# Kernel optimization log

Measured on AMD Instinct MI355X. Metric: run time of the kernel, lower is better.

Reference implementation:

```python
import jax, jax.numpy as jnp
import numpy as np

MEM = 2048

def _linear_params(key, scale):
    kw, kb = jax.random.split(key)
    W = jax.random.uniform(kw, (MEM, MEM), jnp.float32, -scale, scale)
    b = jax.random.uniform(kb, (MEM,), jnp.float32, -scale, scale)
    return W, b

def setup_inputs() -> dict:
    key = jax.random.key(0)
    ks = jax.random.split(key, 18)
    scale = 1.0 / np.sqrt(MEM)
    inp = {
        'lc': jax.random.normal(ks[0], (1, MEM), jnp.float32),
        'lh': jax.random.normal(ks[1], (1, MEM), jnp.float32),
        'rc': jax.random.normal(ks[2], (1, MEM), jnp.float32),
        'rh': jax.random.normal(ks[3], (1, MEM), jnp.float32),
        'S': jax.random.normal(ks[4], (1, MEM), jnp.float32),
        'w': jax.random.normal(ks[5], (1, MEM), jnp.float32),
    }
    names = ['Wh', 'Us', 'ma', 'ilh', 'irh', 'lflh', 'lfrh', 'rflh', 'rfrh', 'ulh', 'urh']
    for i, n in enumerate(names):
        W, b = _linear_params(ks[6 + i], scale)
        inp[n + '_w'] = W
        inp[n + '_b'] = b
    return inp

def _lin(x, W, b):
    return x @ W.T + b

def reference(lc, lh, rc, rh, S, w,
              Wh_w, Wh_b, Us_w, Us_b, ma_w, ma_b,
              ilh_w, ilh_b, irh_w, irh_b,
              lflh_w, lflh_b, lfrh_w, lfrh_b,
              rflh_w, rflh_b, rfrh_w, rfrh_b,
              ulh_w, ulh_b, urh_w, urh_b):
    # attention scoring over the two children
    m_left = jnp.tanh(_lin(lh, Wh_w, Wh_b) + _lin(S, Us_w, Us_b)).squeeze()   # [MEM]
    m_right = jnp.tanh(_lin(rh, Wh_w, Wh_b) + _lin(S, Us_w, Us_b)).squeeze()  # [MEM]
    exp_left = w @ m_left[:, None]    # [1,1]
    exp_right = w @ m_right[:, None]  # [1,1]
    denom = exp_left + exp_right
    left_alpha = exp_left / denom
    right_alpha = exp_right / denom
    # attention-weighted child hidden states
    la = jnp.tanh(_lin(left_alpha * lh, ma_w, ma_b))   # [1,MEM]
    ra = jnp.tanh(_lin(right_alpha * rh, ma_w, ma_b))  # [1,MEM]
    # tree-LSTM gates
    i = jax.nn.sigmoid(_lin(la, ilh_w, ilh_b) + _lin(ra, irh_w, irh_b))
    lf = jax.nn.sigmoid(_lin(la, lflh_w, lflh_b) + _lin(ra, lfrh_w, lfrh_b))
    rf = jax.nn.sigmoid(_lin(la, rflh_w, rflh_b) + _lin(ra, rfrh_w, rfrh_b))
    update = jnp.tanh(_lin(la, ulh_w, ulh_b) + _lin(ra, urh_w, urh_b))
    c = i * update + lf * lc + rf * rc
    h = jnp.tanh(c)
    return (c, h)
```

## Files before the change

kernel.cpp:

```cpp
#include <hip/hip_runtime.h>
#include <hip/hip_bf16.h>
#include <math.h>

#define MEM 2048
#define NF4 512

__device__ __forceinline__ float dot4(float4 a, float4 b) {
    return a.x * b.x + a.y * b.y + a.z * b.z + a.w * b.w;
}

__device__ __forceinline__ float wave_reduce(float v) {
#pragma unroll
    for (int off = 32; off > 0; off >>= 1)
        v += __shfl_down(v, off, 64);
    return v;
}

__device__ __forceinline__ float sigmoidf_(float x) {
    return 1.0f / (1.0f + expf(-x));
}


__global__ __launch_bounds__(256) void
k1_slab(const float* __restrict__ lh, const float* __restrict__ rh,
        const float* __restrict__ S,
        const float* __restrict__ Wh_w, const float* __restrict__ Us_w,
        const float* __restrict__ ma_w,
        float* __restrict__ ws)
{
    __shared__ __align__(16) float s_x1[MEM];
    __shared__ __align__(16) float s_x2[MEM];

    const int t  = threadIdx.x;
    const int m  = blockIdx.y;
    const int rg = blockIdx.x;

    const float* W  = (m == 0) ? Wh_w : (m == 1) ? Us_w : ma_w;
    const float* x1 = (m == 1) ? S : lh;
    const float* x2 = (m == 1) ? S : rh;

    {
        const float4* a4 = (const float4*)x1;
        const float4* b4 = (const float4*)x2;
        float4* s14 = (float4*)s_x1;
        float4* s24 = (float4*)s_x2;
        for (int i = t; i < NF4; i += 256) { s14[i] = a4[i]; s24[i] = b4[i]; }
    }
    __syncthreads();

    const int wv = t >> 6, ln = t & 63;
    const int row0 = rg * 8 + wv * 2;

    const float4* __restrict__ w0 = (const float4*)(W + (size_t)row0 * MEM);
    const float4* __restrict__ w1 = w0 + NF4;
    const float4* sx1 = (const float4*)s_x1;
    const float4* sx2 = (const float4*)s_x2;

    float a00 = 0.f, a01 = 0.f, a10 = 0.f, a11 = 0.f;
#pragma unroll
    for (int i = 0; i < 8; ++i) {
        const int idx = i * 64 + ln;
        const float4 wa = w0[idx];
        const float4 wb = w1[idx];
        const float4 p  = sx1[idx];
        const float4 q  = sx2[idx];
        a00 += dot4(wa, p); a01 += dot4(wa, q);
        a10 += dot4(wb, p); a11 += dot4(wb, q);
    }
    a00 = wave_reduce(a00); a01 = wave_reduce(a01);
    a10 = wave_reduce(a10); a11 = wave_reduce(a11);

    if (ln == 0) {
        if (m == 0) {
            ws[row0] = a00; ws[row0 + 1] = a10;
            ws[MEM + row0] = a01; ws[MEM + row0 + 1] = a11;
        } else if (m == 1) {
            ws[2 * MEM + row0] = a00; ws[2 * MEM + row0 + 1] = a10;
        } else {
            ws[3 * MEM + row0] = a00; ws[3 * MEM + row0 + 1] = a10;
            ws[4 * MEM + row0] = a01; ws[4 * MEM + row0 + 1] = a11;
        }
    }
}

__global__ __launch_bounds__(1024) void
k_mid(const float* __restrict__ w, const float* __restrict__ Wh_b,
      const float* __restrict__ Us_b, const float* __restrict__ ma_b,
      float* __restrict__ ws)
{
    __shared__ float s_red[16][2];
    __shared__ float s_al[2];

    const int t = threadIdx.x;
    float el = 0.f, er = 0.f;
    for (int j = t; j < MEM; j += 1024) {
        const float us = ws[2 * MEM + j] + Us_b[j];
        const float bb = Wh_b[j] + us;
        const float ml = tanhf(ws[j] + bb);
        const float mr = tanhf(ws[MEM + j] + bb);
        const float wj = w[j];
        el += wj * ml; er += wj * mr;
    }
    el = wave_reduce(el);
    er = wave_reduce(er);
    const int wv = t >> 6, ln = t & 63;
    if (ln == 0) { s_red[wv][0] = el; s_red[wv][1] = er; }
    __syncthreads();
    if (t == 0) {
        float e0 = 0.f, e1 = 0.f;
#pragma unroll
        for (int k = 0; k < 16; ++k) { e0 += s_red[k][0]; e1 += s_red[k][1]; }
        const float d = e0 + e1;
        s_al[0] = e0 / d;
        s_al[1] = e1 / d;
    }
    __syncthreads();
    const float al = s_al[0];
    const float ar = s_al[1];
    for (int j = t; j < MEM; j += 1024) {
        const float mb = ma_b[j];
        const float la = tanhf(al * ws[3 * MEM + j] + mb);
        const float ra = tanhf(ar * ws[4 * MEM + j] + mb);
        ws[j] = la;
        ws[MEM + j] = ra;
    }
}

__global__ __launch_bounds__(256) void
k2_slab(const float* __restrict__ ilh_w,  const float* __restrict__ irh_w,
        const float* __restrict__ lflh_w, const float* __restrict__ lfrh_w,
        const float* __restrict__ rflh_w, const float* __restrict__ rfrh_w,
        const float* __restrict__ ulh_w,  const float* __restrict__ urh_w,
        float* __restrict__ ws)
{
    __shared__ __align__(16) float s_x[MEM];

    const int t  = threadIdx.x;
    const int m  = blockIdx.y;
    const int rg = blockIdx.x;

    const float* Wt[8] = {ilh_w, irh_w, lflh_w, lfrh_w, rflh_w, rfrh_w, ulh_w, urh_w};
    const float* W = Wt[m];
    const float* x = ws + (size_t)(m & 1) * MEM;

    {
        const float4* x4 = (const float4*)x;
        float4* s4 = (float4*)s_x;
        for (int i = t; i < NF4; i += 256) s4[i] = x4[i];
    }
    __syncthreads();

    const int wv = t >> 6, ln = t & 63;
    const int row0 = rg * 8 + wv * 2;

    const float4* __restrict__ w0 = (const float4*)(W + (size_t)row0 * MEM);
    const float4* __restrict__ w1 = w0 + NF4;
    const float4* sx = (const float4*)s_x;

    float a0 = 0.f, a1 = 0.f;
#pragma unroll
    for (int i = 0; i < 8; ++i) {
        const int idx = i * 64 + ln;
        const float4 wa = w0[idx];
        const float4 wb = w1[idx];
        const float4 xv = sx[idx];
        a0 += dot4(wa, xv);
        a1 += dot4(wb, xv);
    }
    a0 = wave_reduce(a0);
    a1 = wave_reduce(a1);
    if (ln == 0) {
        float* p = ws + (size_t)(2 + m) * MEM;
        p[row0]     = a0;
        p[row0 + 1] = a1;
    }
}

__global__ __launch_bounds__(256) void
k3_combine(const float* __restrict__ lc, const float* __restrict__ rc,
           const float* __restrict__ ilh_b,  const float* __restrict__ irh_b,
           const float* __restrict__ lflh_b, const float* __restrict__ lfrh_b,
           const float* __restrict__ rflh_b, const float* __restrict__ rfrh_b,
           const float* __restrict__ ulh_b,  const float* __restrict__ urh_b,
           const float* __restrict__ ws, float* __restrict__ out)
{
    const int j = blockIdx.x * 256 + threadIdx.x;
    const float* P = ws + 2 * MEM;
    const float gi = sigmoidf_(P[j]           + P[MEM + j]     + ilh_b[j]  + irh_b[j]);
    const float lf = sigmoidf_(P[2 * MEM + j] + P[3 * MEM + j] + lflh_b[j] + lfrh_b[j]);
    const float rf = sigmoidf_(P[4 * MEM + j] + P[5 * MEM + j] + rflh_b[j] + rfrh_b[j]);
    const float u  = tanhf(    P[6 * MEM + j] + P[7 * MEM + j] + ulh_b[j]  + urh_b[j]);
    const float c  = gi * u + lf * lc[j] + rf * rc[j];
    out[j]       = c;
    out[MEM + j] = tanhf(c);
}

extern "C" void kernel_launch(void* const* d_in, const int* in_sizes, int n_in,
                              void* d_out, int out_size, void* d_ws, size_t ws_size,
                              hipStream_t stream) {
    const float* lc = (const float*)d_in[0];
    const float* lh = (const float*)d_in[1];
    const float* rc = (const float*)d_in[2];
    const float* rh = (const float*)d_in[3];
    const float* S  = (const float*)d_in[4];
    const float* w  = (const float*)d_in[5];
    const float* Wh_w   = (const float*)d_in[6];   const float* Wh_b   = (const float*)d_in[7];
    const float* Us_w   = (const float*)d_in[8];   const float* Us_b   = (const float*)d_in[9];
    const float* ma_w   = (const float*)d_in[10];  const float* ma_b   = (const float*)d_in[11];
    const float* ilh_w  = (const float*)d_in[12];  const float* ilh_b  = (const float*)d_in[13];
    const float* irh_w  = (const float*)d_in[14];  const float* irh_b  = (const float*)d_in[15];
    const float* lflh_w = (const float*)d_in[16];  const float* lflh_b = (const float*)d_in[17];
    const float* lfrh_w = (const float*)d_in[18];  const float* lfrh_b = (const float*)d_in[19];
    const float* rflh_w = (const float*)d_in[20];  const float* rflh_b = (const float*)d_in[21];
    const float* rfrh_w = (const float*)d_in[22];  const float* rfrh_b = (const float*)d_in[23];
    const float* ulh_w  = (const float*)d_in[24];  const float* ulh_b  = (const float*)d_in[25];
    const float* urh_w  = (const float*)d_in[26];  const float* urh_b  = (const float*)d_in[27];

    float* out = (float*)d_out;
    float* ws  = (float*)d_ws;

    dim3 g1(256, 3);
    k1_slab<<<g1, 256, 0, stream>>>(lh, rh, S, Wh_w, Us_w, ma_w, ws);

    k_mid<<<1, 1024, 0, stream>>>(w, Wh_b, Us_b, ma_b, ws);

    dim3 g2(256, 8);
    k2_slab<<<g2, 256, 0, stream>>>(ilh_w, irh_w, lflh_w, lfrh_w,
                                    rflh_w, rfrh_w, ulh_w, urh_w, ws);

    k3_combine<<<8, 256, 0, stream>>>(lc, rc, ilh_b, irh_b, lflh_b, lfrh_b,
                                      rflh_b, rfrh_b, ulh_b, urh_b, ws, out);
}
```

Baseline: 251.3 us.

## Stream weight rows through LDS via async global_load_lds triple buffering

Both matvec kernels now fetch weight rows with global_load_lds straight into a per-wave triple-buffered LDS staging area. Explicit vmcnt waits keep two chunks in flight while the current chunk is consumed. Previously all eight unrolled global loads could already be issued up front, so the aim is mainly to cut register pressure and VGPR round trips. The cost is extra LDS traffic, 24KB more shared memory per block (which may reduce occupancy), and reliance on hand-set wait counts with no barrier.

```diff
diff --git a/kernel.cpp b/kernel.cpp
--- a/kernel.cpp
+++ b/kernel.cpp
@@ -1,6 +1,7 @@
 #include <hip/hip_runtime.h>
 #include <hip/hip_bf16.h>
 #include <math.h>
+#include <stdint.h>
 
 #define MEM 2048
 #define NF4 512
@@ -18,6 +19,18 @@
 
 __device__ __forceinline__ float sigmoidf_(float x) {
     return 1.0f / (1.0f + expf(-x));
+}
+
+__device__ __forceinline__ void dma16(const float* g, float* l) {
+    __builtin_amdgcn_global_load_lds(
+        (const __attribute__((address_space(1))) uint32_t*)(uintptr_t)(const void*)g,
+        (__attribute__((address_space(3))) uint32_t*)(uintptr_t)(const void*)l,
+        16, 0, 0);
+}
+
+template <int N>
+__device__ __forceinline__ void wait_vmcnt() {
+    asm volatile("s_waitcnt vmcnt(%0)" ::"n"(N) : "memory");
 }
 
 
@@ -30,6 +43,7 @@
 {
     __shared__ __align__(16) float s_x1[MEM];
     __shared__ __align__(16) float s_x2[MEM];
+    __shared__ __align__(16) float s_stg[4][3][2][256];
 
     const int t  = threadIdx.x;
     const int m  = blockIdx.y;
@@ -51,19 +65,35 @@
     const int wv = t >> 6, ln = t & 63;
     const int row0 = rg * 8 + wv * 2;
 
-    const float4* __restrict__ w0 = (const float4*)(W + (size_t)row0 * MEM);
-    const float4* __restrict__ w1 = w0 + NF4;
+    const float* g0 = W + (size_t)row0 * MEM + ln * 4;
+    const float* g1 = g0 + MEM;
+
+    dma16(g0 + 0 * 256, &s_stg[wv][0][0][0]);
+    dma16(g1 + 0 * 256, &s_stg[wv][0][1][0]);
+    dma16(g0 + 1 * 256, &s_stg[wv][1][0][0]);
+    dma16(g1 + 1 * 256, &s_stg[wv][1][1][0]);
+
     const float4* sx1 = (const float4*)s_x1;
     const float4* sx2 = (const float4*)s_x2;
 
     float a00 = 0.f, a01 = 0.f, a10 = 0.f, a11 = 0.f;
 #pragma unroll
-    for (int i = 0; i < 8; ++i) {
-        const int idx = i * 64 + ln;
-        const float4 wa = w0[idx];
-        const float4 wb = w1[idx];
-        const float4 p  = sx1[idx];
-        const float4 q  = sx2[idx];
+    for (int c = 0; c < 8; ++c) {
+        if (c + 2 < 8) {
+            const int nb = (c + 2) % 3;
+            dma16(g0 + (c + 2) * 256, &s_stg[wv][nb][0][0]);
+            dma16(g1 + (c + 2) * 256, &s_stg[wv][nb][1][0]);
+            wait_vmcnt<4>();
+        } else if (c + 1 < 8) {
+            wait_vmcnt<2>();
+        } else {
+            wait_vmcnt<0>();
+        }
+        const int buf = c % 3;
+        const float4 wa = ((const float4*)&s_stg[wv][buf][0][0])[ln];
+        const float4 wb = ((const float4*)&s_stg[wv][buf][1][0])[ln];
+        const float4 p  = sx1[c * 64 + ln];
+        const float4 q  = sx2[c * 64 + ln];
         a00 += dot4(wa, p); a01 += dot4(wa, q);
         a10 += dot4(wb, p); a11 += dot4(wb, q);
     }
@@ -134,6 +164,7 @@
         float* __restrict__ ws)
 {
     __shared__ __align__(16) float s_x[MEM];
+    __shared__ __align__(16) float s_stg[4][3][2][256];
 
     const int t  = threadIdx.x;
     const int m  = blockIdx.y;
@@ -153,17 +184,33 @@
     const int wv = t >> 6, ln = t & 63;
     const int row0 = rg * 8 + wv * 2;
 
-    const float4* __restrict__ w0 = (const float4*)(W + (size_t)row0 * MEM);
-    const float4* __restrict__ w1 = w0 + NF4;
+    const float* g0 = W + (size_t)row0 * MEM + ln * 4;
+    const float* g1 = g0 + MEM;
+
+    dma16(g0 + 0 * 256, &s_stg[wv][0][0][0]);
+    dma16(g1 + 0 * 256, &s_stg[wv][0][1][0]);
+    dma16(g0 + 1 * 256, &s_stg[wv][1][0][0]);
+    dma16(g1 + 1 * 256, &s_stg[wv][1][1][0]);
+
     const float4* sx = (const float4*)s_x;
 
     float a0 = 0.f, a1 = 0.f;
 #pragma unroll
-    for (int i = 0; i < 8; ++i) {
-        const int idx = i * 64 + ln;
-        const float4 wa = w0[idx];
-        const float4 wb = w1[idx];
-        const float4 xv = sx[idx];
+    for (int c = 0; c < 8; ++c) {
+        if (c + 2 < 8) {
+            const int nb = (c + 2) % 3;
+            dma16(g0 + (c + 2) * 256, &s_stg[wv][nb][0][0]);
+            dma16(g1 + (c + 2) * 256, &s_stg[wv][nb][1][0]);
+            wait_vmcnt<4>();
+        } else if (c + 1 < 8) {
+            wait_vmcnt<2>();
+        } else {
+            wait_vmcnt<0>();
+        }
+        const int buf = c % 3;
+        const float4 wa = ((const float4*)&s_stg[wv][buf][0][0])[ln];
+        const float4 wb = ((const float4*)&s_stg[wv][buf][1][0])[ln];
+        const float4 xv = sx[c * 64 + ln];
         a0 += dot4(wa, xv);
         a1 += dot4(wb, xv);
     }
```

New measurement: 249.4 us. Within noise of the previous version (-0.8%).
